# Performance work log

Hardware: AMD Instinct MI355X
Metric: run time of the kernel (lower is better)

Reference implementation:

```python
import jax, jax.numpy as jnp
import numpy as np

POS_THR = 0.5
NEG_THR = 0.4
BBOX_STD = np.array([0.1, 0.1, 0.2, 0.2], dtype=np.float32)


def _make_boxes(key, shape, min_sz, max_sz):
    k1, k2, k3, k4 = jax.random.split(key, 4)
    cy = jax.random.uniform(k1, shape, minval=0.2, maxval=0.8)
    cx = jax.random.uniform(k2, shape, minval=0.2, maxval=0.8)
    h = jax.random.uniform(k3, shape, minval=min_sz, maxval=max_sz)
    w = jax.random.uniform(k4, shape, minval=min_sz, maxval=max_sz)
    return jnp.stack([cy - h * 0.5, cx - w * 0.5, cy + h * 0.5, cx + w * 0.5], axis=-1)


def setup_inputs() -> dict:
    key = jax.random.key(0)
    B, G, A = 16, 64, 65536
    kg, ka, kc = jax.random.split(key, 3)
    gt4 = _make_boxes(kg, (B, G), 0.05, 0.4)            # [B,G,4]
    n_valid = 20                                         # first n_valid gts valid, rest pad
    tag = (jnp.arange(G) < n_valid).astype(jnp.float32)
    tag = jnp.broadcast_to(tag, (B, G))
    gt_boxes = jnp.concatenate([gt4, tag[..., None]], axis=-1)          # [B,G,5]
    cls = jax.random.randint(kc, (B, G), 1, 81).astype(jnp.int32)
    gt_class_ids = jnp.stack([cls, tag.astype(jnp.int32)], axis=-1)     # [B,G,2]
    anchors = _make_boxes(ka, (A,), 0.02, 0.5)                          # [A,4]
    return {"gt_boxes": gt_boxes, "gt_class_ids": gt_class_ids, "anchors": anchors}


def _ssd_target(gt_boxes, gt_class_ids, anchors):
    gt = gt_boxes[..., :4]                       # [B,G,4]
    valid = gt_boxes[..., 4] != 0                # [B,G] pad mask (remove_pad equivalent)
    gy1, gx1, gy2, gx2 = (gt[..., i][:, :, None] for i in range(4))  # [B,G,1]
    ay1, ax1, ay2, ax2 = (anchors[:, i][None, None, :] for i in range(4))  # [1,1,A]
    iw = jnp.maximum(0.0, jnp.minimum(gx2, ax2) - jnp.maximum(gx1, ax1))
    ih = jnp.maximum(0.0, jnp.minimum(gy2, ay2) - jnp.maximum(gy1, ay1))
    inter = iw * ih                              # [B,G,A]
    area_gt = (gx2 - gx1) * (gy2 - gy1)
    area_an = (ax2 - ax1) * (ay2 - ay1)
    iou = inter / (area_gt + area_an - inter)    # [B,G,A]
    iou = jnp.where(valid[:, :, None], iou, -1.0)

    iou_max = jnp.max(iou, axis=1)               # [B,A]
    match_idx = jnp.argmax(iou, axis=1)          # [B,A]
    match_gt = jnp.take_along_axis(gt, match_idx[:, :, None], axis=1)   # [B,A,4]
    class_ids = jnp.take_along_axis(gt_class_ids[..., 0], match_idx, axis=1)  # [B,A]

    anchors_tag = jnp.where(iou_max >= POS_THR, 1.0,
                            jnp.where(iou_max < NEG_THR, -1.0, 0.0))    # [B,A]

    h = anchors[:, 2] - anchors[:, 0]            # [A]
    w = anchors[:, 3] - anchors[:, 1]
    cy = (anchors[:, 2] + anchors[:, 0]) * 0.5
    cx = (anchors[:, 3] + anchors[:, 1]) * 0.5
    gh = match_gt[..., 2] - match_gt[..., 0]     # [B,A]
    gw = match_gt[..., 3] - match_gt[..., 1]
    gcy = (match_gt[..., 2] + match_gt[..., 0]) * 0.5
    gcx = (match_gt[..., 3] + match_gt[..., 1]) * 0.5
    dy = (gcy - cy) / h
    dx = (gcx - cx) / w
    dh = jnp.log(gh / h)
    dw = jnp.log(gw / w)
    deltas = jnp.stack([dy, dx, dh, dw], axis=-1) / jnp.asarray(BBOX_STD)  # [B,A,4]
    return deltas, class_ids, anchors_tag


def reference(gt_boxes, gt_class_ids, anchors):
    return _ssd_target(gt_boxes, gt_class_ids, anchors)
```

## Files before the change

kernel.cpp:

```cpp
#include <hip/hip_runtime.h>

#define G 64
#define K 2
#define POS_THR 0.5f
#define NEG_THR 0.4f

__global__ __launch_bounds__(256) void ssd_target_kernel(
    const float* __restrict__ gt_boxes,
    const int*   __restrict__ gt_class,
    const float* __restrict__ anchors,
    float* __restrict__ out,
    int A, int B)
{
    __shared__ float4 s_box[G];
    __shared__ float  s_area[G], s_cls[G];
    __shared__ int    s_nv;

    const int b = blockIdx.y;

    if (threadIdx.x < G) {
        const int g = threadIdx.x;
        const float* p = gt_boxes + ((size_t)b * G + g) * 5;
        const float y1 = p[0], x1 = p[1], y2 = p[2], x2 = p[3], tagv = p[4];
        const bool valid = (tagv != 0.0f);
        const unsigned long long m = __ballot(valid);
        const int pos = __popcll(m & ((1ull << g) - 1ull));
        const float cls = (float)gt_class[((size_t)b * G + g) * 2 + 0];
        if (valid) {
            s_box[pos] = make_float4(y1, x1, y2, x2);
            s_area[pos] = (x2 - x1) * (y2 - y1);
            s_cls[pos]  = cls;
        }
        if (g == 0) {
            s_nv = __popcll(m);
            if (m == 0ull) {
                s_box[0] = make_float4(y1, x1, y2, x2);
                s_cls[0] = cls;
            }
        }
    }
    __syncthreads();

    const int t  = threadIdx.x;
    const int a0 = blockIdx.x * (256 * K) + t;

    float4 an[K];
    float  area_an[K];
    #pragma unroll
    for (int k = 0; k < K; ++k) {
        an[k] = reinterpret_cast<const float4*>(anchors)[a0 + k * 256];
        area_an[k] = (an[k].w - an[k].y) * (an[k].z - an[k].x);
    }

    const int nv = s_nv;
    float best[K], second[K];
    int   bg[K];
    #pragma unroll
    for (int k = 0; k < K; ++k) { best[k] = -1.0f; second[k] = -1.0f; bg[k] = 0; }

    #pragma unroll 4
    for (int i = 0; i < nv; ++i) {
        const float4 gb = s_box[i];
        const float  ga = s_area[i];
        #pragma unroll
        for (int k = 0; k < K; ++k) {
            float iw = fmaxf(0.0f, fminf(gb.w, an[k].w) - fmaxf(gb.y, an[k].y));
            float ih = fmaxf(0.0f, fminf(gb.z, an[k].z) - fmaxf(gb.x, an[k].x));
            float inter = iw * ih;
            float denom = ga + area_an[k] - inter;
            float apx = inter * __builtin_amdgcn_rcpf(denom);
            bg[k]     = (apx > best[k]) ? i : bg[k];
            second[k] = __builtin_amdgcn_fmed3f(second[k], apx, best[k]);
            best[k]   = fmaxf(best[k], apx);
        }
    }

    #pragma unroll
    for (int k = 0; k < K; ++k) {
        const float ay1 = an[k].x, ax1 = an[k].y, ay2 = an[k].z, ax2 = an[k].w;
        int   win = bg[k];
        float q;
        if (nv == 0) {
            q = -1.0f; win = 0;
        } else {
            const bool need_exact =
                (best[k] > 0.0f) && (second[k] >= best[k] * (1.0f - 1e-5f));
            if (need_exact) {
                float be = -1.0f; int bi = 0;
                for (int i = 0; i < nv; ++i) {
                    const float4 gb = s_box[i];
                    float iw = fmaxf(0.0f, fminf(gb.w, ax2) - fmaxf(gb.y, ax1));
                    float ih = fmaxf(0.0f, fminf(gb.z, ay2) - fmaxf(gb.x, ay1));
                    float inter = iw * ih;
                    float denom = s_area[i] + area_an[k] - inter;
                    float iou = inter / denom;
                    if (iou > be) { be = iou; bi = i; }
                }
                q = be; win = bi;
            } else {
                const float4 gb = s_box[win];
                float iw = fmaxf(0.0f, fminf(gb.w, ax2) - fmaxf(gb.y, ax1));
                float ih = fmaxf(0.0f, fminf(gb.z, ay2) - fmaxf(gb.x, ay1));
                float inter = iw * ih;
                float denom = s_area[win] + area_an[k] - inter;
                q = inter / denom;
            }
        }

        const float4 gb = s_box[win];
        const float h  = ay2 - ay1;
        const float w  = ax2 - ax1;
        const float rh = __builtin_amdgcn_rcpf(h);
        const float rw = __builtin_amdgcn_rcpf(w);
        const float cy = (ay2 + ay1) * 0.5f;
        const float cx = (ax2 + ax1) * 0.5f;
        const float gh  = gb.z - gb.x;
        const float gw  = gb.w - gb.y;
        const float gcy = (gb.z + gb.x) * 0.5f;
        const float gcx = (gb.w + gb.y) * 0.5f;

        const float dy = (gcy - cy) * rh * 10.0f;
        const float dx = (gcx - cx) * rw * 10.0f;
        const float dh = __log2f(gh * rh) * 3.4657359028f;
        const float dw = __log2f(gw * rw) * 3.4657359028f;

        const float tag = (q >= POS_THR) ? 1.0f : ((q < NEG_THR) ? -1.0f : 0.0f);

        const size_t idx = (size_t)b * A + (size_t)(a0 + k * 256);
        float4 d; d.x = dy; d.y = dx; d.z = dh; d.w = dw;
        reinterpret_cast<float4*>(out)[idx] = d;
        out[(size_t)B * A * 4 + idx] = s_cls[win];
        out[(size_t)B * A * 5 + idx] = tag;
    }
}

extern "C" void kernel_launch(void* const* d_in, const int* in_sizes, int n_in,
                              void* d_out, int out_size, void* d_ws, size_t ws_size,
                              hipStream_t stream) {
    const float* gt_boxes = (const float*)d_in[0];
    const int*   gt_class = (const int*)d_in[1];
    const float* anchors  = (const float*)d_in[2];
    float* out = (float*)d_out;

    const int B = in_sizes[0] / (G * 5);
    const int A = in_sizes[2] / 4;

    dim3 grid(A / (256 * K), B);
    dim3 block(256);
    ssd_target_kernel<<<grid, block, 0, stream>>>(gt_boxes, gt_class, anchors, out, A, B);
}
```

Before: 78.32 us.

## Precompute compacted GT table in separate kernel, read via scalar loads, raise K to 4

Moves the per-batch compaction of valid ground-truth boxes into a small prepass kernel that writes boxes, areas and classes to a global workspace. The main kernel reads the table straight from global memory in its IoU loop. The loads are uniform across the block, so they can go through scalar or cached loads. The shared-memory copy and its barrier now come after the main loop and serve only the rare exact-recheck path, and anchors per thread rise from 2 to 4. The cost is an extra kernel launch and a global workspace sized for at most 32 batches. Doubling K also raises register pressure and halves the number of blocks.

New measurement: 79.91 us. 1.02x slower.

```diff
diff --git a/kernel.cpp b/kernel.cpp
--- a/kernel.cpp
+++ b/kernel.cpp
@@ -1,47 +1,52 @@
 #include <hip/hip_runtime.h>
 
 #define G 64
-#define K 2
+#define K 4
 #define POS_THR 0.5f
 #define NEG_THR 0.4f
+#define WB_STRIDE 512
+
+__device__ float g_ws[32 * WB_STRIDE];
+
+__global__ __launch_bounds__(64) void compact_kernel(
+    const float* __restrict__ gt_boxes,
+    const int*   __restrict__ gt_class)
+{
+    const int b = blockIdx.x;
+    const int g = threadIdx.x;
+    const float* p = gt_boxes + ((size_t)b * G + g) * 5;
+    const float y1 = p[0], x1 = p[1], y2 = p[2], x2 = p[3], tagv = p[4];
+    const bool valid = (tagv != 0.0f);
+    const unsigned long long m = __ballot(valid);
+    const int pos = __popcll(m & ((1ull << g) - 1ull));
+    const float cls = (float)gt_class[((size_t)b * G + g) * 2 + 0];
+    float* wb = g_ws + (size_t)b * WB_STRIDE;
+    if (valid) {
+        reinterpret_cast<float4*>(wb)[pos] = make_float4(y1, x1, y2, x2);
+        reinterpret_cast<float2*>(wb + 256)[pos] = make_float2((x2 - x1) * (y2 - y1), cls);
+    }
+    if (g == 0) {
+        reinterpret_cast<int*>(wb + 384)[0] = __popcll(m);
+        if (m == 0ull) {
+            reinterpret_cast<float4*>(wb)[0] = make_float4(y1, x1, y2, x2);
+            reinterpret_cast<float2*>(wb + 256)[0] = make_float2(0.0f, cls);
+        }
+    }
+}
 
 __global__ __launch_bounds__(256) void ssd_target_kernel(
-    const float* __restrict__ gt_boxes,
-    const int*   __restrict__ gt_class,
     const float* __restrict__ anchors,
     float* __restrict__ out,
     int A, int B)
 {
-    __shared__ float4 s_box[G];
-    __shared__ float  s_area[G], s_cls[G];
-    __shared__ int    s_nv;
+    __shared__ float s_ws[G * 6];
 
     const int b = blockIdx.y;
+    const float* __restrict__ wb = g_ws + (size_t)b * WB_STRIDE;
 
-    if (threadIdx.x < G) {
-        const int g = threadIdx.x;
-        const float* p = gt_boxes + ((size_t)b * G + g) * 5;
-        const float y1 = p[0], x1 = p[1], y2 = p[2], x2 = p[3], tagv = p[4];
-        const bool valid = (tagv != 0.0f);
-        const unsigned long long m = __ballot(valid);
-        const int pos = __popcll(m & ((1ull << g) - 1ull));
-        const float cls = (float)gt_class[((size_t)b * G + g) * 2 + 0];
-        if (valid) {
-            s_box[pos] = make_float4(y1, x1, y2, x2);
-            s_area[pos] = (x2 - x1) * (y2 - y1);
-            s_cls[pos]  = cls;
-        }
-        if (g == 0) {
-            s_nv = __popcll(m);
-            if (m == 0ull) {
-                s_box[0] = make_float4(y1, x1, y2, x2);
-                s_cls[0] = cls;
-            }
-        }
-    }
-    __syncthreads();
+    const int t = threadIdx.x;
+    for (int j = t; j < 384; j += 256) s_ws[j] = wb[j];
 
-    const int t  = threadIdx.x;
     const int a0 = blockIdx.x * (256 * K) + t;
 
     float4 an[K];
@@ -52,7 +57,8 @@
         area_an[k] = (an[k].w - an[k].y) * (an[k].z - an[k].x);
     }
 
-    const int nv = s_nv;
+    const int nv = reinterpret_cast<const int*>(wb + 384)[0];
+
     float best[K], second[K];
     int   bg[K];
     #pragma unroll
@@ -60,8 +66,8 @@
 
     #pragma unroll 4
     for (int i = 0; i < nv; ++i) {
-        const float4 gb = s_box[i];
-        const float  ga = s_area[i];
+        const float4 gb = reinterpret_cast<const float4*>(wb)[i];
+        const float  ga = reinterpret_cast<const float2*>(wb + 256)[i].x;
         #pragma unroll
         for (int k = 0; k < K; ++k) {
             float iw = fmaxf(0.0f, fminf(gb.w, an[k].w) - fmaxf(gb.y, an[k].y));
@@ -74,6 +80,11 @@
             best[k]   = fmaxf(best[k], apx);
         }
     }
+
+    __syncthreads();
+
+    const float4* s_box = reinterpret_cast<const float4*>(s_ws);
+    const float2* s_ac  = reinterpret_cast<const float2*>(s_ws + 256);
 
     #pragma unroll
     for (int k = 0; k < K; ++k) {
@@ -92,7 +103,7 @@
                     float iw = fmaxf(0.0f, fminf(gb.w, ax2) - fmaxf(gb.y, ax1));
                     float ih = fmaxf(0.0f, fminf(gb.z, ay2) - fmaxf(gb.x, ay1));
                     float inter = iw * ih;
-                    float denom = s_area[i] + area_an[k] - inter;
+                    float denom = s_ac[i].x + area_an[k] - inter;
                     float iou = inter / denom;
                     if (iou > be) { be = iou; bi = i; }
                 }
@@ -102,7 +113,7 @@
                 float iw = fmaxf(0.0f, fminf(gb.w, ax2) - fmaxf(gb.y, ax1));
                 float ih = fmaxf(0.0f, fminf(gb.z, ay2) - fmaxf(gb.x, ay1));
                 float inter = iw * ih;
-                float denom = s_area[win] + area_an[k] - inter;
+                float denom = s_ac[win].x + area_an[k] - inter;
                 q = inter / denom;
             }
         }
@@ -129,7 +140,7 @@
         const size_t idx = (size_t)b * A + (size_t)(a0 + k * 256);
         float4 d; d.x = dy; d.y = dx; d.z = dh; d.w = dw;
         reinterpret_cast<float4*>(out)[idx] = d;
-        out[(size_t)B * A * 4 + idx] = s_cls[win];
+        out[(size_t)B * A * 4 + idx] = s_ac[win].y;
         out[(size_t)B * A * 5 + idx] = tag;
     }
 }
@@ -145,7 +156,9 @@
     const int B = in_sizes[0] / (G * 5);
     const int A = in_sizes[2] / 4;
 
+    compact_kernel<<<dim3(B), dim3(64), 0, stream>>>(gt_boxes, gt_class);
+
     dim3 grid(A / (256 * K), B);
     dim3 block(256);
-    ssd_target_kernel<<<grid, block, 0, stream>>>(gt_boxes, gt_class, anchors, out, A, B);
+    ssd_target_kernel<<<grid, block, 0, stream>>>(anchors, out, A, B);
 }
```
